# Optimization experiments

Measured on AMD Instinct MI355X. Metric: run time of the kernel, lower is better.

The kernel has to match this reference:

```python
import jax, jax.numpy as jnp
import numpy as np

H_DIM = 32
EPS = 1e-7


def setup_inputs() -> dict:
    key = jax.random.key(0)
    ks = jax.random.split(key, 9)
    B, L, I = 2048, 256, 8
    return {
        "X": jax.random.normal(ks[0], (B, L, I), dtype=jnp.float32),
        "y": jax.random.randint(ks[1], (B,), 0, 2, dtype=jnp.int64),
        "W1": jax.random.normal(ks[2], (I, H_DIM), dtype=jnp.float32),
        "cls_tok": jax.random.normal(ks[3], (H_DIM,), dtype=jnp.float32),
        "W_q": jax.random.normal(ks[4], (H_DIM, H_DIM), dtype=jnp.float32),
        "W_k": jax.random.normal(ks[5], (H_DIM, H_DIM), dtype=jnp.float32),
        "W_v": jax.random.normal(ks[6], (H_DIM, H_DIM), dtype=jnp.float32),
        "W_t": jax.random.normal(ks[7], (H_DIM, H_DIM), dtype=jnp.float32),
        "W2": jax.random.normal(ks[8], (H_DIM, 2), dtype=jnp.float32),
    }


def reference(X, y, W1, cls_tok, W_q, W_k, W_v, W_t, W2):
    B = X.shape[0]
    # global mean/std normalization (torch.std is unbiased, ddof=1)
    h_pre1 = (X - X.mean()) / (X.std(ddof=1) + EPS)
    h_1 = h_pre1 @ W1                                   # [B, L, H]
    cls = jnp.broadcast_to(cls_tok[None, None, :], (B, 1, H_DIM))
    h_pre2 = jnp.concatenate([h_1, cls], axis=1)        # [B, L+1, H]
    Q = h_pre2 @ W_q
    K = h_pre2 @ W_k
    V = h_pre2 @ W_v
    S = jax.nn.softmax(jnp.einsum('bqh,bkh->bqk', Q, K) / jnp.sqrt(jnp.float32(H_DIM)), axis=-1)
    h_2 = jnp.einsum('bqk,bkh->bqh', S, V) + h_pre2 @ W_t
    z = h_2[:, -1] @ W2                                 # [B, o_dim]
    log_s = jax.nn.log_softmax(z, axis=-1)
    loss = -jnp.take_along_axis(log_s, y[:, None], axis=1)[:, 0].mean()
    return loss
```

## Files before the change

kernel.cpp:

```cpp
#include <hip/hip_runtime.h>

#define N_TOTAL 4194304
#define B_SIZE  2048
#define L_SIZE  256
#define I_DIM   8
#define H       32
#define K1_BLK  256

#define CRAW_OFF 4096
#define LOSS_OFF 4128

__global__ __launch_bounds__(1024) void k1_stats(
    const float4* __restrict__ X4,
    const float* __restrict__ W1, const float* __restrict__ cls,
    const float* __restrict__ Wq, const float* __restrict__ Wk,
    const float* __restrict__ Wv, const float* __restrict__ Wt,
    const float* __restrict__ W2, double* __restrict__ dws)
{
    const int t = threadIdx.x, b = blockIdx.x;
    const int lane = t & 63, wid = t >> 6;
    const int g = b * 1024 + t;

    float s1 = 0.f, s2 = 0.f;
    #pragma unroll
    for (int i = 0; i < 4; i++) {
        float4 v = X4[g + i * 262144];
        s1 += v.x + v.y + v.z + v.w;
        s2 += v.x * v.x + v.y * v.y + v.z * v.z + v.w * v.w;
    }
    for (int off = 32; off; off >>= 1) {
        s1 += __shfl_down(s1, off);
        s2 += __shfl_down(s2, off);
    }
    __shared__ float a1[16], a2[16];
    if (lane == 0) { a1[wid] = s1; a2[wid] = s2; }
    __syncthreads();
    if (t == 0) {
        float r1 = 0.f, r2 = 0.f;
        #pragma unroll
        for (int i = 0; i < 16; i++) { r1 += a1[i]; r2 += a2[i]; }
        dws[16 * b]     = (double)r1;
        dws[16 * b + 1] = (double)r2;
    }

    if (b == 0) {
        __shared__ float qv[H], kcls[H], vcls[H], tv[H], gg[H], WV[I_DIM][H];
        const float rs32 = 0.17677669529663687f;
        float* craw = (float*)(dws + CRAW_OFF);
        if (t < H) {
            const int h = t;
            float q_ = 0.f, k_ = 0.f, v_ = 0.f, t_ = 0.f;
            for (int j = 0; j < H; j++) {
                float cj = cls[j];
                q_ += cj * Wq[j * H + h];
                k_ += cj * Wk[j * H + h];
                v_ += cj * Wv[j * H + h];
                t_ += cj * Wt[j * H + h];
            }
            qv[h] = q_; kcls[h] = k_; vcls[h] = v_; tv[h] = t_;
        }
        __syncthreads();
        if (t < H) {
            const int h = t;
            float g_ = 0.f;
            for (int j = 0; j < H; j++) g_ += Wk[h * H + j] * qv[j];
            gg[h] = g_;
            for (int i = 0; i < I_DIM; i++) {
                float a = 0.f;
                for (int j = 0; j < H; j++) a += W1[i * H + j] * Wv[j * H + h];
                WV[i][h] = a;
            }
        }
        __syncthreads();
        if (t < I_DIM) {
            float a = 0.f;
            for (int j = 0; j < H; j++) a += W1[t * H + j] * gg[j];
            craw[t] = a;
        }
        if (t < I_DIM * 2) {
            const int i = t >> 1, o = t & 1;
            float a = 0.f;
            for (int j = 0; j < H; j++) a += WV[i][j] * W2[j * 2 + o];
            craw[10 + i * 2 + o] = a;
        }
        if (t == 0) {
            float c2 = 0.f;
            for (int j = 0; j < H; j++) c2 += qv[j] * kcls[j];
            craw[9] = c2 * rs32;
            float vw0 = 0.f, vw1 = 0.f, tw0 = 0.f, tw1 = 0.f;
            for (int j = 0; j < H; j++) {
                vw0 += vcls[j] * W2[j * 2];     vw1 += vcls[j] * W2[j * 2 + 1];
                tw0 += tv[j]   * W2[j * 2];     tw1 += tv[j]   * W2[j * 2 + 1];
            }
            craw[28] = vw0; craw[29] = vw1; craw[30] = tw0; craw[31] = tw1;
        }
    }
}

__global__ __launch_bounds__(256) void k2_attn(
    const float* __restrict__ X, const int* __restrict__ y,
    double* __restrict__ dws)
{
    const int t = threadIdx.x, b = blockIdx.x;
    const int lane = t & 63, wid = t >> 6;

    const float4* Xb = (const float4*)(X + (size_t)b * (L_SIZE * I_DIM));
    float4 p0 = Xb[2 * t], p1 = Xb[2 * t + 1];
    float x[8] = {p0.x, p0.y, p0.z, p0.w, p1.x, p1.y, p1.z, p1.w};

    double d1 = dws[16 * t], d2 = dws[16 * t + 1];
    for (int off = 32; off; off >>= 1) {
        d1 += __shfl_down(d1, off);
        d2 += __shfl_down(d2, off);
    }
    __shared__ double da[4], db[4];
    if (lane == 0) { da[wid] = d1; db[wid] = d2; }
    __syncthreads();

    __shared__ float sNegMu, sSdev;
    if (t == 0) {
        double S1 = da[0] + da[1] + da[2] + da[3];
        double S2 = db[0] + db[1] + db[2] + db[3];
        double mu = S1 / (double)N_TOTAL;
        double var = (S2 - S1 * S1 / (double)N_TOTAL) / (double)(N_TOTAL - 1);
        sSdev = (float)(sqrt(var) + 1e-7);
        sNegMu = (float)(-mu);
    }
    __syncthreads();

    __shared__ float cst[32];
    const float* craw = (const float*)(dws + CRAW_OFF);
    const float rs32 = 0.17677669529663687f;
    if (t < 32) {
        const float sdev = sSdev, negmu = sNegMu;
        if (t < 8) {
            cst[t] = craw[t] / sdev * rs32;
        } else if (t == 8) {
            float cs = 0.f;
            for (int i = 0; i < 8; i++) cs += craw[i] / sdev * rs32;
            cst[8] = negmu * cs;
        } else if (t == 9) {
            cst[9] = craw[9];
        } else if (t < 26) {
            cst[t] = craw[t] / sdev;
        } else if (t == 26) {
            float m0 = 0.f;
            for (int i = 0; i < 8; i++) m0 += craw[10 + 2 * i] / sdev;
            cst[26] = negmu * m0;
        } else if (t == 27) {
            float m1 = 0.f;
            for (int i = 0; i < 8; i++) m1 += craw[11 + 2 * i] / sdev;
            cst[27] = negmu * m1;
        } else {
            cst[t] = craw[t];
        }
    }
    __syncthreads();

    float sc = cst[8];
    #pragma unroll
    for (int i = 0; i < 8; i++) sc += x[i] * cst[i];

    float m = sc;
    for (int off = 32; off; off >>= 1) m = fmaxf(m, __shfl_down(m, off));
    __shared__ float wmax[4];
    __shared__ float wsum[4][9];
    if (lane == 0) wmax[wid] = m;
    __syncthreads();
    m = fmaxf(fmaxf(wmax[0], wmax[1]), fmaxf(wmax[2], wmax[3]));
    m = fmaxf(m, cst[9]);

    float e = expf(sc - m);
    float v[9];
    v[0] = e;
    #pragma unroll
    for (int i = 0; i < 8; i++) v[i + 1] = e * x[i];
    for (int off = 32; off; off >>= 1) {
        #pragma unroll
        for (int j = 0; j < 9; j++) v[j] += __shfl_down(v[j], off);
    }
    if (lane == 0) {
        #pragma unroll
        for (int j = 0; j < 9; j++) wsum[wid][j] = v[j];
    }
    __syncthreads();

    if (t == 0) {
        float se = wsum[0][0] + wsum[1][0] + wsum[2][0] + wsum[3][0];
        float ecls = expf(cst[9] - m);
        float inv = 1.f / (se + ecls);
        float S256 = ecls * inv;
        float z[2];
        #pragma unroll
        for (int o = 0; o < 2; o++) {
            float a = 0.f;
            #pragma unroll
            for (int i = 0; i < 8; i++) {
                float wi = (wsum[0][i + 1] + wsum[1][i + 1] +
                            wsum[2][i + 1] + wsum[3][i + 1]) * inv;
                a += wi * cst[10 + i * 2 + o];
            }
            z[o] = a + (1.f - S256) * cst[26 + o] + S256 * cst[28 + o] + cst[30 + o];
        }
        float zm = fmaxf(z[0], z[1]);
        float lse = zm + logf(expf(z[0] - zm) + expf(z[1] - zm));
        int yb = y[b];
        dws[LOSS_OFF + b] = (double)(lse - z[yb]);
    }
}

__global__ __launch_bounds__(256) void k3_finalize(
    const double* __restrict__ dws, float* __restrict__ out)
{
    const int t = threadIdx.x;
    const int lane = t & 63, wid = t >> 6;
    double l = 0.0;
    for (int i = t; i < B_SIZE; i += 256) l += dws[LOSS_OFF + i];
    for (int off = 32; off; off >>= 1) l += __shfl_down(l, off);
    __shared__ double da[4];
    if (lane == 0) da[wid] = l;
    __syncthreads();
    if (t == 0)
        out[0] = (float)((da[0] + da[1] + da[2] + da[3]) / (double)B_SIZE);
}

extern "C" void kernel_launch(void* const* d_in, const int* in_sizes, int n_in,
                              void* d_out, int out_size, void* d_ws, size_t ws_size,
                              hipStream_t stream) {
    const float* X   = (const float*)d_in[0];
    const int*   y   = (const int*)d_in[1];
    const float* W1  = (const float*)d_in[2];
    const float* cls = (const float*)d_in[3];
    const float* Wq  = (const float*)d_in[4];
    const float* Wk  = (const float*)d_in[5];
    const float* Wv  = (const float*)d_in[6];
    const float* Wt  = (const float*)d_in[7];
    const float* W2  = (const float*)d_in[8];
    float* out = (float*)d_out;
    double* dws = (double*)d_ws;

    hipLaunchKernelGGL(k1_stats, dim3(K1_BLK), dim3(1024), 0, stream,
                       (const float4*)X, W1, cls, Wq, Wk, Wv, Wt, W2, dws);
    hipLaunchKernelGGL(k2_attn, dim3(B_SIZE), dim3(256), 0, stream, X, y, dws);
    hipLaunchKernelGGL(k3_finalize, dim3(1), dim3(256), 0, stream, dws, out);
}
```

Before: 26.55 us.

## Process one batch row per wavefront and fuse finalize via fixed-point atomic counter

Restructures k2 so that each 512-thread block handles 8 batch rows, one per wavefront. Each lane processes 4 sequence positions, so the per-row softmax reductions need only wave shuffles and no block barriers. The separate finalize kernel is removed: each block converts its summed loss to 32.32 fixed point and atomically adds it into a counter whose top byte counts arriving blocks, and the last block writes the mean. This removes one launch and many block-level syncs, and cuts the number of blocks doing the redundant stats/constant setup from 2048 to 256. In exchange it relies on fixed-point atomics, which assume the loss is non-negative and fits in the range, and on the counter being zeroed by k1.

```diff
diff --git a/kernel.cpp b/kernel.cpp
--- a/kernel.cpp
+++ b/kernel.cpp
@@ -8,7 +8,9 @@
 #define K1_BLK  256
 
 #define CRAW_OFF 4096
-#define LOSS_OFF 4128
+#define ACC_OFF  4112
+#define FIXSCALE 4294967296.0
+#define MASK56   0x00FFFFFFFFFFFFFFull
 
 __global__ __launch_bounds__(1024) void k1_stats(
     const float4* __restrict__ X4,
@@ -93,46 +95,41 @@
                 tw0 += tv[j]   * W2[j * 2];     tw1 += tv[j]   * W2[j * 2 + 1];
             }
             craw[28] = vw0; craw[29] = vw1; craw[30] = tw0; craw[31] = tw1;
+            *(unsigned long long*)(dws + ACC_OFF) = 0ull;
         }
     }
 }
 
-__global__ __launch_bounds__(256) void k2_attn(
+__global__ __launch_bounds__(512) void k2_attn(
     const float* __restrict__ X, const int* __restrict__ y,
-    double* __restrict__ dws)
+    double* __restrict__ dws, float* __restrict__ out)
 {
     const int t = threadIdx.x, b = blockIdx.x;
-    const int lane = t & 63, wid = t >> 6;
-
-    const float4* Xb = (const float4*)(X + (size_t)b * (L_SIZE * I_DIM));
-    float4 p0 = Xb[2 * t], p1 = Xb[2 * t + 1];
-    float x[8] = {p0.x, p0.y, p0.z, p0.w, p1.x, p1.y, p1.z, p1.w};
-
-    double d1 = dws[16 * t], d2 = dws[16 * t + 1];
-    for (int off = 32; off; off >>= 1) {
-        d1 += __shfl_down(d1, off);
-        d2 += __shfl_down(d2, off);
-    }
+    const int lane = t & 63, w = t >> 6;
+
     __shared__ double da[4], db[4];
-    if (lane == 0) { da[wid] = d1; db[wid] = d2; }
-    __syncthreads();
-
-    __shared__ float sNegMu, sSdev;
-    if (t == 0) {
-        double S1 = da[0] + da[1] + da[2] + da[3];
-        double S2 = db[0] + db[1] + db[2] + db[3];
-        double mu = S1 / (double)N_TOTAL;
-        double var = (S2 - S1 * S1 / (double)N_TOTAL) / (double)(N_TOTAL - 1);
-        sSdev = (float)(sqrt(var) + 1e-7);
-        sNegMu = (float)(-mu);
-    }
-    __syncthreads();
-
     __shared__ float cst[32];
+    __shared__ double wloss[8];
+
+    if (t < 256) {
+        double d1 = dws[16 * t], d2 = dws[16 * t + 1];
+        for (int off = 32; off; off >>= 1) {
+            d1 += __shfl_down(d1, off);
+            d2 += __shfl_down(d2, off);
+        }
+        if (lane == 0) { da[w] = d1; db[w] = d2; }
+    }
+    __syncthreads();
+    const double S1 = da[0] + da[1] + da[2] + da[3];
+    const double S2 = db[0] + db[1] + db[2] + db[3];
+    const double mu = S1 / (double)N_TOTAL;
+    const double var = (S2 - S1 * S1 / (double)N_TOTAL) / (double)(N_TOTAL - 1);
+    const float sdev = (float)(sqrt(var) + 1e-7);
+    const float negmu = (float)(-mu);
+
     const float* craw = (const float*)(dws + CRAW_OFF);
     const float rs32 = 0.17677669529663687f;
     if (t < 32) {
-        const float sdev = sSdev, negmu = sNegMu;
         if (t < 8) {
             cst[t] = craw[t] / sdev * rs32;
         } else if (t == 8) {
@@ -157,36 +154,44 @@
     }
     __syncthreads();
 
-    float sc = cst[8];
-    #pragma unroll
-    for (int i = 0; i < 8; i++) sc += x[i] * cst[i];
-
-    float m = sc;
-    for (int off = 32; off; off >>= 1) m = fmaxf(m, __shfl_down(m, off));
-    __shared__ float wmax[4];
-    __shared__ float wsum[4][9];
-    if (lane == 0) wmax[wid] = m;
-    __syncthreads();
-    m = fmaxf(fmaxf(wmax[0], wmax[1]), fmaxf(wmax[2], wmax[3]));
+    const int r = b * 8 + w;
+    const float4* Xb = (const float4*)(X + (size_t)r * (L_SIZE * I_DIM));
+    float x[4][8];
+    float sc[4];
+    const float c8 = cst[8];
+    float u0 = cst[0], u1 = cst[1], u2 = cst[2], u3 = cst[3];
+    float u4 = cst[4], u5 = cst[5], u6 = cst[6], u7 = cst[7];
+    #pragma unroll
+    for (int j = 0; j < 4; j++) {
+        const int p = 64 * j + lane;
+        float4 p0 = Xb[2 * p], p1 = Xb[2 * p + 1];
+        x[j][0] = p0.x; x[j][1] = p0.y; x[j][2] = p0.z; x[j][3] = p0.w;
+        x[j][4] = p1.x; x[j][5] = p1.y; x[j][6] = p1.z; x[j][7] = p1.w;
+        sc[j] = c8 + x[j][0] * u0 + x[j][1] * u1 + x[j][2] * u2 + x[j][3] * u3
+                   + x[j][4] * u4 + x[j][5] * u5 + x[j][6] * u6 + x[j][7] * u7;
+    }
+
+    float m = fmaxf(fmaxf(sc[0], sc[1]), fmaxf(sc[2], sc[3]));
+    for (int off = 32; off; off >>= 1) m = fmaxf(m, __shfl_xor(m, off));
     m = fmaxf(m, cst[9]);
 
-    float e = expf(sc - m);
     float v[9];
-    v[0] = e;
-    #pragma unroll
-    for (int i = 0; i < 8; i++) v[i + 1] = e * x[i];
+    #pragma unroll
+    for (int j2 = 0; j2 < 9; j2++) v[j2] = 0.f;
+    #pragma unroll
+    for (int j = 0; j < 4; j++) {
+        float e = expf(sc[j] - m);
+        v[0] += e;
+        #pragma unroll
+        for (int i = 0; i < 8; i++) v[i + 1] += e * x[j][i];
+    }
     for (int off = 32; off; off >>= 1) {
         #pragma unroll
-        for (int j = 0; j < 9; j++) v[j] += __shfl_down(v[j], off);
-    }
+        for (int j2 = 0; j2 < 9; j2++) v[j2] += __shfl_down(v[j2], off);
+    }
+
     if (lane == 0) {
-        #pragma unroll
-        for (int j = 0; j < 9; j++) wsum[wid][j] = v[j];
-    }
-    __syncthreads();
-
-    if (t == 0) {
-        float se = wsum[0][0] + wsum[1][0] + wsum[2][0] + wsum[3][0];
+        float se = v[0];
         float ecls = expf(cst[9] - m);
         float inv = 1.f / (se + ecls);
         float S256 = ecls * inv;
@@ -195,33 +200,31 @@
         for (int o = 0; o < 2; o++) {
             float a = 0.f;
             #pragma unroll
-            for (int i = 0; i < 8; i++) {
-                float wi = (wsum[0][i + 1] + wsum[1][i + 1] +
-                            wsum[2][i + 1] + wsum[3][i + 1]) * inv;
-                a += wi * cst[10 + i * 2 + o];
-            }
+            for (int i = 0; i < 8; i++)
+                a += (v[i + 1] * inv) * cst[10 + i * 2 + o];
             z[o] = a + (1.f - S256) * cst[26 + o] + S256 * cst[28 + o] + cst[30 + o];
         }
         float zm = fmaxf(z[0], z[1]);
         float lse = zm + logf(expf(z[0] - zm) + expf(z[1] - zm));
-        int yb = y[b];
-        dws[LOSS_OFF + b] = (double)(lse - z[yb]);
-    }
-}
-
-__global__ __launch_bounds__(256) void k3_finalize(
-    const double* __restrict__ dws, float* __restrict__ out)
-{
-    const int t = threadIdx.x;
-    const int lane = t & 63, wid = t >> 6;
-    double l = 0.0;
-    for (int i = t; i < B_SIZE; i += 256) l += dws[LOSS_OFF + i];
-    for (int off = 32; off; off >>= 1) l += __shfl_down(l, off);
-    __shared__ double da[4];
-    if (lane == 0) da[wid] = l;
-    __syncthreads();
-    if (t == 0)
-        out[0] = (float)((da[0] + da[1] + da[2] + da[3]) / (double)B_SIZE);
+        int yb = y[r];
+        wloss[w] = (double)(lse - z[yb]);
+    }
+    __syncthreads();
+
+    if (t == 0) {
+        double blockloss = 0.0;
+        #pragma unroll
+        for (int i = 0; i < 8; i++) blockloss += wloss[i];
+        unsigned long long fixed =
+            (unsigned long long)(blockloss * FIXSCALE + 0.5);
+        unsigned long long* acc = (unsigned long long*)(dws + ACC_OFF);
+        unsigned long long old = __hip_atomic_fetch_add(
+            acc, fixed + (1ull << 56), __ATOMIC_RELAXED, __HIP_MEMORY_SCOPE_AGENT);
+        if ((old >> 56) == 255ull) {
+            unsigned long long total = ((old & MASK56) + fixed) & MASK56;
+            out[0] = (float)((double)total / FIXSCALE / (double)B_SIZE);
+        }
+    }
 }
 
 extern "C" void kernel_launch(void* const* d_in, const int* in_sizes, int n_in,
@@ -241,6 +244,6 @@
 
     hipLaunchKernelGGL(k1_stats, dim3(K1_BLK), dim3(1024), 0, stream,
                        (const float4*)X, W1, cls, Wq, Wk, Wv, Wt, W2, dws);
-    hipLaunchKernelGGL(k2_attn, dim3(B_SIZE), dim3(256), 0, stream, X, y, dws);
-    hipLaunchKernelGGL(k3_finalize, dim3(1), dim3(256), 0, stream, dws, out);
+    hipLaunchKernelGGL(k2_attn, dim3(K1_BLK), dim3(512), 0, stream,
+                       X, y, dws, out);
 }
```

Result: faster. 21.72 us (-18.2%).
